# Optimization experiments

Measured on AMD Instinct MI355X. Metric: run time of the kernel, lower is better.

Reference implementation:

```python
import jax, jax.numpy as jnp
import numpy as np

N = 50000
E = 800000
FEAT, COND, HID, LAT = 64, 32, 64, 32


def gcn_conv(x, W, b, src, dst, n):
    xw = x @ W  # [N, out]
    deg = jnp.zeros((n,), xw.dtype).at[dst].add(1.0) + 1.0  # in-degree + self loop
    dinv = jax.lax.rsqrt(deg)
    coef = dinv[src] * dinv[dst]  # [E]
    msg = xw[src] * coef[:, None]  # gather + scale
    agg = jax.ops.segment_sum(msg, dst, num_segments=n)
    agg = agg + xw * (1.0 / deg)[:, None]  # self-loop contribution
    return agg + b


def setup_inputs() -> dict:
    key = jax.random.key(0)
    ks = jax.random.split(key, 12)
    s = 0.05
    return {
        "feature": jax.random.normal(ks[0], (N, FEAT), jnp.float32),
        "condition": jax.random.normal(ks[1], (N, COND), jnp.float32),
        "edge_index": jax.random.randint(ks[2], (2, E), 0, N, jnp.int64),
        "enc_i2h_W": jax.random.normal(ks[3], (FEAT + COND, HID), jnp.float32) * s,
        "enc_i2h_b": jnp.zeros((HID,), jnp.float32),
        "enc_mean_W": jax.random.normal(ks[4], (HID, LAT), jnp.float32) * s,
        "enc_mean_b": jnp.zeros((LAT,), jnp.float32),
        "enc_logvar_W": jax.random.normal(ks[5], (HID, LAT), jnp.float32) * s,
        "enc_logvar_b": jnp.zeros((LAT,), jnp.float32),
        "dec_i2h_W": jax.random.normal(ks[6], (LAT + COND, HID), jnp.float32) * s,
        "dec_i2h_b": jnp.zeros((HID,), jnp.float32),
        "dec_out_W": jax.random.normal(ks[7], (HID, FEAT), jnp.float32) * s,
        "dec_out_b": jnp.zeros((FEAT,), jnp.float32),
    }


def reference(feature, condition, edge_index,
              enc_i2h_W, enc_i2h_b, enc_mean_W, enc_mean_b,
              enc_logvar_W, enc_logvar_b,
              dec_i2h_W, dec_i2h_b, dec_out_W, dec_out_b):
    src, dst = edge_index[0], edge_index[1]
    n = feature.shape[0]
    # encoder
    x = jnp.concatenate([feature, condition], axis=1)
    h = jax.nn.relu(gcn_conv(x, enc_i2h_W, enc_i2h_b, src, dst, n))
    mean = gcn_conv(h, enc_mean_W, enc_mean_b, src, dst, n)
    logvar = gcn_conv(h, enc_logvar_W, enc_logvar_b, src, dst, n)
    noise = jax.random.normal(jax.random.key(42), logvar.shape, logvar.dtype)
    z = noise * jnp.exp(0.5 * logvar) + mean
    # decoder
    xd = jnp.concatenate([z, condition], axis=1)
    hd = jax.nn.relu(gcn_conv(xd, dec_i2h_W, dec_i2h_b, src, dst, n))
    out = gcn_conv(hd, dec_out_W, dec_out_b, src, dst, n)
    return (z, mean, logvar, out)
```

## Files before the change

### kernel.cpp

```cpp
#include <hip/hip_runtime.h>
#include <hip/hip_bf16.h>
#include <hip/hip_fp16.h>
#include <math.h>


static __device__ __forceinline__ unsigned rotl32(unsigned x, int d) {
  return (x << d) | (x >> (32 - d));
}

static __device__ __forceinline__ void threefry_0_42(unsigned& x0, unsigned& x1) {
  const unsigned ks0 = 0u, ks1 = 42u, ks2 = 0u ^ 42u ^ 0x1BD11BDAu;
  x0 += ks0; x1 += ks1;
#define TF_R(r) { x0 += x1; x1 = rotl32(x1, (r)); x1 ^= x0; }
  TF_R(13) TF_R(15) TF_R(26) TF_R(6)
  x0 += ks1; x1 += ks2 + 1u;
  TF_R(17) TF_R(29) TF_R(16) TF_R(24)
  x0 += ks2; x1 += ks0 + 2u;
  TF_R(13) TF_R(15) TF_R(26) TF_R(6)
  x0 += ks0; x1 += ks1 + 3u;
  TF_R(17) TF_R(29) TF_R(16) TF_R(24)
  x0 += ks1; x1 += ks2 + 4u;
  TF_R(13) TF_R(15) TF_R(26) TF_R(6)
  x0 += ks2; x1 += ks0 + 5u;
#undef TF_R
}

static __device__ __forceinline__ float erfinv_f(float u) {
  float w = -logf((1.0f - u) * (1.0f + u));
  float p;
  if (w < 5.0f) {
    w = w - 2.5f;
    p = 2.81022636e-08f;
    p = fmaf(p, w, 3.43273939e-07f);
    p = fmaf(p, w, -3.5233877e-06f);
    p = fmaf(p, w, -4.39150654e-06f);
    p = fmaf(p, w, 0.00021858087f);
    p = fmaf(p, w, -0.00125372503f);
    p = fmaf(p, w, -0.00417768164f);
    p = fmaf(p, w, 0.246640727f);
    p = fmaf(p, w, 1.50140941f);
  } else {
    w = sqrtf(w) - 3.0f;
    p = -0.000200214257f;
    p = fmaf(p, w, 0.000100950558f);
    p = fmaf(p, w, 0.00134934322f);
    p = fmaf(p, w, -0.00367342844f);
    p = fmaf(p, w, 0.00573950773f);
    p = fmaf(p, w, -0.0076224613f);
    p = fmaf(p, w, 0.00943887047f);
    p = fmaf(p, w, 1.00167406f);
    p = fmaf(p, w, 2.83297682f);
  }
  return p * u;
}

static __device__ __forceinline__ float jax_normal_at(unsigned j) {
  unsigned x0 = 0u, x1 = j;
  threefry_0_42(x0, x1);
  unsigned bits = x0 ^ x1;
  float f = __uint_as_float((bits >> 9) | 0x3f800000u) - 1.0f;
  float u = fmaf(f, 1.99999994f, -0.99999994f);
  return 1.41421356237f * erfinv_f(u);
}


__global__ void zero_i_kernel(int* __restrict__ p, int n) {
  int i = blockIdx.x * blockDim.x + threadIdx.x;
  if (i < n) p[i] = 0;
}

__global__ void degree_i_kernel(const int* __restrict__ dstI, int* __restrict__ cnt, int ne) {
  int e = blockIdx.x * blockDim.x + threadIdx.x;
  if (e < ne) atomicAdd(&cnt[dstI[e]], 1);
}

__global__ __launch_bounds__(256) void scan1_kernel(const int* __restrict__ cnt,
                                                    int* __restrict__ rowptr,
                                                    int* __restrict__ bsum, int n) {
  __shared__ int s[256];
  const int t = threadIdx.x;
  const int base = blockIdx.x * 1024 + t * 4;
  int v0, v1, v2, v3;
  if (base + 3 < n) {
    int4 v = *(const int4*)(cnt + base);
    v0 = v.x; v1 = v.y; v2 = v.z; v3 = v.w;
  } else {
    v0 = (base + 0 < n) ? cnt[base + 0] : 0;
    v1 = (base + 1 < n) ? cnt[base + 1] : 0;
    v2 = (base + 2 < n) ? cnt[base + 2] : 0;
    v3 = (base + 3 < n) ? cnt[base + 3] : 0;
  }
  int tot = v0 + v1 + v2 + v3;
  s[t] = tot;
  __syncthreads();
  for (int off = 1; off < 256; off <<= 1) {
    int x = (t >= off) ? s[t - off] : 0;
    __syncthreads();
    s[t] += x;
    __syncthreads();
  }
  int excl = s[t] - tot;
  if (t == 255) bsum[blockIdx.x] = s[t];
  if (base + 0 < n) rowptr[base + 0] = excl;
  if (base + 1 < n) rowptr[base + 1] = excl + v0;
  if (base + 2 < n) rowptr[base + 2] = excl + v0 + v1;
  if (base + 3 < n) rowptr[base + 3] = excl + v0 + v1 + v2;
}

__global__ __launch_bounds__(256) void scanP_kernel(int* __restrict__ bsum,
                                                    int* __restrict__ boff,
                                                    int nb, int* __restrict__ rowptr,
                                                    int n, int ne) {
  __shared__ int s[256];
  const int t = threadIdx.x;
  int v = (t < nb) ? bsum[t] : 0;
  s[t] = v;
  __syncthreads();
  for (int off = 1; off < 256; off <<= 1) {
    int x = (t >= off) ? s[t - off] : 0;
    __syncthreads();
    s[t] += x;
    __syncthreads();
  }
  if (t < nb) boff[t] = s[t] - v;
  if (t == 0) rowptr[n] = ne;
}

__global__ void scan2_kernel(int* __restrict__ rowptr, const int* __restrict__ boff,
                             int* __restrict__ cnt, float* __restrict__ dinv, int n) {
  int i = blockIdx.x * blockDim.x + threadIdx.x;
  if (i < n) {
    rowptr[i] += boff[i >> 10];
    float d = (float)cnt[i] + 1.0f;
    dinv[i] = 1.0f / sqrtf(d);
    cnt[i] = 0;
  }
}

__global__ void fill_kernel(const int* __restrict__ srcI, const int* __restrict__ dstI,
                            const int* __restrict__ rowptr, int* __restrict__ cnt,
                            unsigned short* __restrict__ ssrc, int ne) {
  int e = blockIdx.x * blockDim.x + threadIdx.x;
  if (e >= ne) return;
  int s = srcI[e], d = dstI[e];
  int pos = rowptr[d] + atomicAdd(&cnt[d], 1);
  ssrc[pos] = (unsigned short)s;
}

struct alignas(16) half8 { __half h[8]; };

template<int IN1, int IN2, bool DUALW>
__global__ __launch_bounds__(256) void gemm_kernel(
    const float* __restrict__ X1, const float* __restrict__ X2,
    const float* __restrict__ Wa, const float* __restrict__ Wb,
    const float* __restrict__ dinv, __half* __restrict__ Y, int n) {
  constexpr int IN = IN1 + IN2;
  constexpr int IP = IN + 4;
  __shared__ float xs[128 * IP];
  __shared__ float ws[IN * 64];

  const int tid = threadIdx.x;
  const int base = blockIdx.x * 128;

  for (int i = tid; i < IN * 64; i += 256) {
    if (DUALW) {
      int k = i >> 6, c = i & 63;
      ws[i] = (c < 32) ? Wa[k * 32 + c] : Wb[k * 32 + (c - 32)];
    } else {
      ws[i] = Wa[i];
    }
  }
  for (int idx = tid; idx < 128 * (IN1 / 4); idx += 256) {
    int node = idx / (IN1 / 4);
    int k4 = (idx % (IN1 / 4)) * 4;
    int g = base + node;
    float4 v = (g < n) ? *(const float4*)(X1 + (size_t)g * IN1 + k4)
                       : make_float4(0.f, 0.f, 0.f, 0.f);
    *(float4*)&xs[node * IP + k4] = v;
  }
  if (IN2 > 0) {
    for (int idx = tid; idx < 128 * (IN2 / 4); idx += 256) {
      int node = idx / (IN2 / 4);
      int k4 = (idx % (IN2 / 4)) * 4;
      int g = base + node;
      float4 v = (g < n) ? *(const float4*)(X2 + (size_t)g * IN2 + k4)
                         : make_float4(0.f, 0.f, 0.f, 0.f);
      *(float4*)&xs[node * IP + IN1 + k4] = v;
    }
  }
  __syncthreads();

  const int c8 = (tid & 7) * 8;
  const int r4 = (tid >> 3) * 4;
  float acc[4][8];
#pragma unroll
  for (int i = 0; i < 4; ++i)
#pragma unroll
    for (int c = 0; c < 8; ++c) acc[i][c] = 0.0f;

#pragma unroll 2
  for (int kk = 0; kk < IN; kk += 4) {
    float4 xv[4];
    float4 wv[4][2];
#pragma unroll
    for (int i = 0; i < 4; ++i) xv[i] = *(const float4*)&xs[(r4 + i) * IP + kk];
#pragma unroll
    for (int j = 0; j < 4; ++j) {
      wv[j][0] = *(const float4*)&ws[(kk + j) * 64 + c8];
      wv[j][1] = *(const float4*)&ws[(kk + j) * 64 + c8 + 4];
    }
#pragma unroll
    for (int i = 0; i < 4; ++i) {
      const float* xi = (const float*)&xv[i];
#pragma unroll
      for (int j = 0; j < 4; ++j) {
        const float* wj = (const float*)&wv[j][0];
#pragma unroll
        for (int c = 0; c < 8; ++c) {
          acc[i][c] = fmaf(xi[j], wj[c], acc[i][c]);
        }
      }
    }
  }

#pragma unroll
  for (int i = 0; i < 4; ++i) {
    int g = base + r4 + i;
    if (g < n) {
      float dv = dinv[g];
      half8 o;
#pragma unroll
      for (int c = 0; c < 8; ++c) o.h[c] = __float2half(acc[i][c] * dv);
      *(half8*)&Y[(size_t)g * 64 + c8] = o;
    }
  }
}

template<int MODE>
__global__ __launch_bounds__(256) void gather_kernel(
    const int* __restrict__ rowptr, const unsigned short* __restrict__ ssrc,
    const __half* __restrict__ xwp, const float* __restrict__ dinv,
    const float* __restrict__ b0, const float* __restrict__ b1,
    float* __restrict__ out, int n) {
  const int node = (blockIdx.x * 256 + threadIdx.x) >> 6;
  const int lane = threadIdx.x & 63;
  if (node >= n) return;
  const int hf = lane >> 5;
  const int cl = lane & 31;

  float2 a1, a2, a3, a4;
  a2.x = a2.y = a3.x = a3.y = a4.x = a4.y = 0.f;
  {
    float2 f = __half22float2(((const __half2*)(xwp + (size_t)node * 64))[cl]);
    a1.x = hf ? 0.f : f.x;
    a1.y = hf ? 0.f : f.y;
  }

  const int beg = rowptr[node];
  const int end = rowptr[node + 1];
  for (int cbase = beg; cbase < end; cbase += 64) {
    int m = end - cbase; if (m > 64) m = 64;
    unsigned sv = (lane < m) ? (unsigned)ssrc[cbase + lane] : 0u;
    int k = 0;
    for (; k + 7 < m; k += 8) {
      unsigned sa = __shfl(sv, k + 0 + hf, 64);
      unsigned sb = __shfl(sv, k + 2 + hf, 64);
      unsigned sc = __shfl(sv, k + 4 + hf, 64);
      unsigned sd = __shfl(sv, k + 6 + hf, 64);
      float2 fa = __half22float2(((const __half2*)(xwp + (size_t)sa * 64))[cl]);
      float2 fb = __half22float2(((const __half2*)(xwp + (size_t)sb * 64))[cl]);
      float2 fc = __half22float2(((const __half2*)(xwp + (size_t)sc * 64))[cl]);
      float2 fd = __half22float2(((const __half2*)(xwp + (size_t)sd * 64))[cl]);
      a1.x += fa.x; a1.y += fa.y;
      a2.x += fb.x; a2.y += fb.y;
      a3.x += fc.x; a3.y += fc.y;
      a4.x += fd.x; a4.y += fd.y;
    }
    for (; k + 1 < m; k += 2) {
      unsigned sa = __shfl(sv, k + hf, 64);
      float2 fa = __half22float2(((const __half2*)(xwp + (size_t)sa * 64))[cl]);
      a1.x += fa.x; a1.y += fa.y;
    }
    if (k < m) {
      unsigned sa = __shfl(sv, k, 64);
      if (hf == 0) {
        float2 fa = __half22float2(((const __half2*)(xwp + (size_t)sa * 64))[cl]);
        a1.x += fa.x; a1.y += fa.y;
      }
    }
  }
  float2 acc;
  acc.x = (a1.x + a2.x) + (a3.x + a4.x);
  acc.y = (a1.y + a2.y) + (a3.y + a4.y);
  acc.x += __shfl(acc.x, lane ^ 32, 64);
  acc.y += __shfl(acc.y, lane ^ 32, 64);
  float dv = dinv[node];
  float vx = acc.x * dv, vy = acc.y * dv;

  if (hf != 0) return;

  const int c0 = 2 * cl;
  if (MODE == 0) {
    float2 o;
    o.x = fmaxf(vx + b0[c0], 0.0f);
    o.y = fmaxf(vy + b0[c0 + 1], 0.0f);
    ((float2*)(out + (size_t)node * 64))[cl] = o;
  } else if (MODE == 2) {
    float2 o;
    o.x = vx + b0[c0];
    o.y = vy + b0[c0 + 1];
    ((float2*)(out + (size_t)node * 64))[cl] = o;
  } else {
    float bx = (c0 < 32) ? b0[c0] : b1[c0 - 32];
    float by = (c0 + 1 < 32) ? b0[c0 + 1] : b1[c0 + 1 - 32];
    vx += bx; vy += by;
    float ox = __shfl(vx, lane + 16, 64);
    float oy = __shfl(vy, lane + 16, 64);
    const int NZ = n * 32;
    if (cl < 16) {
      int j = node * 32 + c0;
      float n0 = jax_normal_at((unsigned)j);
      float n1 = jax_normal_at((unsigned)(j + 1));
      out[j]     = fmaf(n0, expf(0.5f * ox), vx);
      out[j + 1] = fmaf(n1, expf(0.5f * oy), vy);
      out[NZ + j]     = vx;
      out[NZ + j + 1] = vy;
    } else {
      int j = node * 32 + (c0 - 32);
      out[2 * NZ + j]     = vx;
      out[2 * NZ + j + 1] = vy;
    }
  }
}


extern "C" void kernel_launch(void* const* d_in, const int* in_sizes, int n_in,
                              void* d_out, int out_size, void* d_ws, size_t ws_size,
                              hipStream_t stream) {
  const float* feat = (const float*)d_in[0];
  const float* cond = (const float*)d_in[1];
  const int*   eidx = (const int*)d_in[2];
  const float* W1  = (const float*)d_in[3];
  const float* b1  = (const float*)d_in[4];
  const float* Wm  = (const float*)d_in[5];
  const float* bm  = (const float*)d_in[6];
  const float* Wlv = (const float*)d_in[7];
  const float* blv = (const float*)d_in[8];
  const float* Wd  = (const float*)d_in[9];
  const float* bd  = (const float*)d_in[10];
  const float* Wo  = (const float*)d_in[11];
  const float* bo  = (const float*)d_in[12];

  const int n  = in_sizes[0] / 64;
  const int ne = in_sizes[2] / 2;
  const int* srcI = eidx;
  const int* dstI = eidx + ne;

  int*   cnt    = (int*)d_ws;
  int*   rowptr = cnt + n;
  int*   bsum   = rowptr + n + 1;
  int*   boff   = bsum + 256;
  float* dinv   = (float*)(boff + 256);
  __half* xwp   = (__half*)(dinv + n);
  float* h      = (float*)(xwp + (size_t)n * 64);
  unsigned short* ssrc = (unsigned short*)(h + (size_t)n * 64);

  float* dout   = (float*)d_out;
  float* zbuf   = dout;
  float* outbuf = dout + (size_t)3 * n * 32;

  const int BT = 256;
  auto blk = [](long long t) { return (int)((t + 255) / 256); };
  const int nb_n  = blk(n);
  const int nb_e  = blk(ne);
  const int nb_sc = (n + 1023) / 1024;
  const int nb_gw = blk((long long)n * 64);
  const int nb_g  = (n + 127) / 128;

  hipLaunchKernelGGL(zero_i_kernel, dim3(nb_n), dim3(BT), 0, stream, cnt, n);
  hipLaunchKernelGGL(degree_i_kernel, dim3(nb_e), dim3(BT), 0, stream, dstI, cnt, ne);
  hipLaunchKernelGGL(scan1_kernel, dim3(nb_sc), dim3(BT), 0, stream, cnt, rowptr, bsum, n);
  hipLaunchKernelGGL(scanP_kernel, dim3(1), dim3(BT), 0, stream, bsum, boff, nb_sc, rowptr, n, ne);
  hipLaunchKernelGGL(scan2_kernel, dim3(nb_n), dim3(BT), 0, stream, rowptr, boff, cnt, dinv, n);
  hipLaunchKernelGGL(fill_kernel, dim3(nb_e), dim3(BT), 0, stream,
                     srcI, dstI, rowptr, cnt, ssrc, ne);

  hipLaunchKernelGGL((gemm_kernel<64, 32, false>), dim3(nb_g), dim3(BT), 0, stream,
                     feat, cond, W1, nullptr, dinv, xwp, n);
  hipLaunchKernelGGL((gather_kernel<0>), dim3(nb_gw), dim3(BT), 0, stream,
                     rowptr, ssrc, xwp, dinv, b1, nullptr, h, n);

  hipLaunchKernelGGL((gemm_kernel<64, 0, true>), dim3(nb_g), dim3(BT), 0, stream,
                     h, nullptr, Wm, Wlv, dinv, xwp, n);
  hipLaunchKernelGGL((gather_kernel<1>), dim3(nb_gw), dim3(BT), 0, stream,
                     rowptr, ssrc, xwp, dinv, bm, blv, dout, n);

  hipLaunchKernelGGL((gemm_kernel<32, 32, false>), dim3(nb_g), dim3(BT), 0, stream,
                     zbuf, cond, Wd, nullptr, dinv, xwp, n);
  hipLaunchKernelGGL((gather_kernel<0>), dim3(nb_gw), dim3(BT), 0, stream,
                     rowptr, ssrc, xwp, dinv, bd, nullptr, h, n);

  hipLaunchKernelGGL((gemm_kernel<64, 0, false>), dim3(nb_g), dim3(BT), 0, stream,
                     h, nullptr, Wo, nullptr, dinv, xwp, n);
  hipLaunchKernelGGL((gather_kernel<2>), dim3(nb_gw), dim3(BT), 0, stream,
                     rowptr, ssrc, xwp, dinv, bo, nullptr, outbuf, n);
}
```

Measured before the change: 273.3 us.

## Use fp16 MFMA for node GEMMs and store hidden activations in fp16

Replaces the scalar FMA register-tiled GEMM with an MFMA 16x16x32 fp16 kernel. Inputs and a transposed weight tile are staged in LDS as fp16. The hidden activations h written by the ReLU gather are now stored as fp16, which halves their write and read traffic, and the next GEMM loads them directly. The output stores become scattered per-element half writes rather than 16-byte vectors, and inputs lose precision by being rounded to fp16. dinv is offset by 3 ints, likely to keep later buffers aligned for vector loads.

```diff
diff --git a/kernel.cpp b/kernel.cpp
--- a/kernel.cpp
+++ b/kernel.cpp
@@ -2,6 +2,10 @@
 #include <hip/hip_bf16.h>
 #include <hip/hip_fp16.h>
 #include <math.h>
+
+typedef _Float16 f16;
+typedef __attribute__((ext_vector_type(8))) _Float16 f16x8;
+typedef __attribute__((ext_vector_type(4))) float f32x4;
 
 
 static __device__ __forceinline__ unsigned rotl32(unsigned x, int d) {
@@ -147,36 +151,47 @@
   ssrc[pos] = (unsigned short)s;
 }
 
-struct alignas(16) half8 { __half h[8]; };
-
-template<int IN1, int IN2, bool DUALW>
-__global__ __launch_bounds__(256) void gemm_kernel(
-    const float* __restrict__ X1, const float* __restrict__ X2,
+template<int IN1, int IN2, bool X1HALF, bool DUALW>
+__global__ __launch_bounds__(256) void gemm_mfma_kernel(
+    const void* __restrict__ X1v, const float* __restrict__ X2,
     const float* __restrict__ Wa, const float* __restrict__ Wb,
     const float* __restrict__ dinv, __half* __restrict__ Y, int n) {
   constexpr int IN = IN1 + IN2;
-  constexpr int IP = IN + 4;
-  __shared__ float xs[128 * IP];
-  __shared__ float ws[IN * 64];
+  constexpr int IP = IN + 8;
+  __shared__ f16 xs[128 * IP];
+  __shared__ f16 wt[64 * IP];
 
   const int tid = threadIdx.x;
   const int base = blockIdx.x * 128;
 
   for (int i = tid; i < IN * 64; i += 256) {
-    if (DUALW) {
-      int k = i >> 6, c = i & 63;
-      ws[i] = (c < 32) ? Wa[k * 32 + c] : Wb[k * 32 + (c - 32)];
-    } else {
-      ws[i] = Wa[i];
-    }
-  }
-  for (int idx = tid; idx < 128 * (IN1 / 4); idx += 256) {
-    int node = idx / (IN1 / 4);
-    int k4 = (idx % (IN1 / 4)) * 4;
-    int g = base + node;
-    float4 v = (g < n) ? *(const float4*)(X1 + (size_t)g * IN1 + k4)
-                       : make_float4(0.f, 0.f, 0.f, 0.f);
-    *(float4*)&xs[node * IP + k4] = v;
+    int k = i >> 6, c = i & 63;
+    float w;
+    if (DUALW) w = (c < 32) ? Wa[k * 32 + c] : Wb[k * 32 + (c - 32)];
+    else       w = Wa[i];
+    wt[c * IP + k] = (f16)w;
+  }
+  if (X1HALF) {
+    const __half* X1 = (const __half*)X1v;
+    for (int idx = tid; idx < 128 * (IN1 / 8); idx += 256) {
+      int node = idx / (IN1 / 8);
+      int k8 = (idx % (IN1 / 8)) * 8;
+      int g = base + node;
+      f16x8 v = {};
+      if (g < n) v = *(const f16x8*)(X1 + (size_t)g * IN1 + k8);
+      *(f16x8*)&xs[node * IP + k8] = v;
+    }
+  } else {
+    const float* X1 = (const float*)X1v;
+    for (int idx = tid; idx < 128 * (IN1 / 4); idx += 256) {
+      int node = idx / (IN1 / 4);
+      int k4 = (idx % (IN1 / 4)) * 4;
+      int g = base + node;
+      float4 v = (g < n) ? *(const float4*)(X1 + (size_t)g * IN1 + k4)
+                         : make_float4(0.f, 0.f, 0.f, 0.f);
+      f16* p = &xs[node * IP + k4];
+      p[0] = (f16)v.x; p[1] = (f16)v.y; p[2] = (f16)v.z; p[3] = (f16)v.w;
+    }
   }
   if (IN2 > 0) {
     for (int idx = tid; idx < 128 * (IN2 / 4); idx += 256) {
@@ -185,53 +200,44 @@
       int g = base + node;
       float4 v = (g < n) ? *(const float4*)(X2 + (size_t)g * IN2 + k4)
                          : make_float4(0.f, 0.f, 0.f, 0.f);
-      *(float4*)&xs[node * IP + IN1 + k4] = v;
+      f16* p = &xs[node * IP + IN1 + k4];
+      p[0] = (f16)v.x; p[1] = (f16)v.y; p[2] = (f16)v.z; p[3] = (f16)v.w;
     }
   }
   __syncthreads();
 
-  const int c8 = (tid & 7) * 8;
-  const int r4 = (tid >> 3) * 4;
-  float acc[4][8];
+  const int wid  = tid >> 6;
+  const int lane = tid & 63;
+  const int l15  = lane & 15;
+  const int lk8  = (lane >> 4) * 8;
+
+  f32x4 acc[2][4] = {{{0.f,0.f,0.f,0.f}}};
+  constexpr int KB = IN / 32;
 #pragma unroll
-  for (int i = 0; i < 4; ++i)
+  for (int kb = 0; kb < KB; ++kb) {
+    const int k0 = kb * 32 + lk8;
+    f16x8 a0 = *(const f16x8*)&xs[(wid * 32 +      l15) * IP + k0];
+    f16x8 a1 = *(const f16x8*)&xs[(wid * 32 + 16 + l15) * IP + k0];
 #pragma unroll
-    for (int c = 0; c < 8; ++c) acc[i][c] = 0.0f;
-
-#pragma unroll 2
-  for (int kk = 0; kk < IN; kk += 4) {
-    float4 xv[4];
-    float4 wv[4][2];
+    for (int ct = 0; ct < 4; ++ct) {
+      f16x8 b = *(const f16x8*)&wt[(ct * 16 + l15) * IP + k0];
+      acc[0][ct] = __builtin_amdgcn_mfma_f32_16x16x32_f16(a0, b, acc[0][ct], 0, 0, 0);
+      acc[1][ct] = __builtin_amdgcn_mfma_f32_16x16x32_f16(a1, b, acc[1][ct], 0, 0, 0);
+    }
+  }
+
 #pragma unroll
-    for (int i = 0; i < 4; ++i) xv[i] = *(const float4*)&xs[(r4 + i) * IP + kk];
-#pragma unroll
-    for (int j = 0; j < 4; ++j) {
-      wv[j][0] = *(const float4*)&ws[(kk + j) * 64 + c8];
-      wv[j][1] = *(const float4*)&ws[(kk + j) * 64 + c8 + 4];
-    }
+  for (int rt = 0; rt < 2; ++rt) {
 #pragma unroll
     for (int i = 0; i < 4; ++i) {
-      const float* xi = (const float*)&xv[i];
+      int node = base + wid * 32 + rt * 16 + (lane >> 4) * 4 + i;
+      if (node < n) {
+        float dv = dinv[node];
 #pragma unroll
-      for (int j = 0; j < 4; ++j) {
-        const float* wj = (const float*)&wv[j][0];
-#pragma unroll
-        for (int c = 0; c < 8; ++c) {
-          acc[i][c] = fmaf(xi[j], wj[c], acc[i][c]);
+        for (int ct = 0; ct < 4; ++ct) {
+          Y[(size_t)node * 64 + ct * 16 + l15] = __float2half(acc[rt][ct][i] * dv);
         }
       }
-    }
-  }
-
-#pragma unroll
-  for (int i = 0; i < 4; ++i) {
-    int g = base + r4 + i;
-    if (g < n) {
-      float dv = dinv[g];
-      half8 o;
-#pragma unroll
-      for (int c = 0; c < 8; ++c) o.h[c] = __float2half(acc[i][c] * dv);
-      *(half8*)&Y[(size_t)g * 64 + c8] = o;
     }
   }
 }
@@ -241,7 +247,7 @@
     const int* __restrict__ rowptr, const unsigned short* __restrict__ ssrc,
     const __half* __restrict__ xwp, const float* __restrict__ dinv,
     const float* __restrict__ b0, const float* __restrict__ b1,
-    float* __restrict__ out, int n) {
+    void* __restrict__ outv, int n) {
   const int node = (blockIdx.x * 256 + threadIdx.x) >> 6;
   const int lane = threadIdx.x & 63;
   if (node >= n) return;
@@ -301,16 +307,17 @@
 
   const int c0 = 2 * cl;
   if (MODE == 0) {
-    float2 o;
-    o.x = fmaxf(vx + b0[c0], 0.0f);
-    o.y = fmaxf(vy + b0[c0 + 1], 0.0f);
-    ((float2*)(out + (size_t)node * 64))[cl] = o;
+    __half* out = (__half*)outv;
+    __half2 o = __floats2half2_rn(fmaxf(vx + b0[c0], 0.0f), fmaxf(vy + b0[c0 + 1], 0.0f));
+    ((__half2*)(out + (size_t)node * 64))[cl] = o;
   } else if (MODE == 2) {
+    float* out = (float*)outv;
     float2 o;
     o.x = vx + b0[c0];
     o.y = vy + b0[c0 + 1];
     ((float2*)(out + (size_t)node * 64))[cl] = o;
   } else {
+    float* out = (float*)outv;
     float bx = (c0 < 32) ? b0[c0] : b1[c0 - 32];
     float by = (c0 + 1 < 32) ? b0[c0 + 1] : b1[c0 + 1 - 32];
     vx += bx; vy += by;
@@ -360,9 +367,9 @@
   int*   rowptr = cnt + n;
   int*   bsum   = rowptr + n + 1;
   int*   boff   = bsum + 256;
-  float* dinv   = (float*)(boff + 256);
+  float* dinv   = (float*)(boff + 256 + 3);
   __half* xwp   = (__half*)(dinv + n);
-  float* h      = (float*)(xwp + (size_t)n * 64);
+  __half* h     = xwp + (size_t)n * 64;
   unsigned short* ssrc = (unsigned short*)(h + (size_t)n * 64);
 
   float* dout   = (float*)d_out;
@@ -385,22 +392,22 @@
   hipLaunchKernelGGL(fill_kernel, dim3(nb_e), dim3(BT), 0, stream,
                      srcI, dstI, rowptr, cnt, ssrc, ne);
 
-  hipLaunchKernelGGL((gemm_kernel<64, 32, false>), dim3(nb_g), dim3(BT), 0, stream,
+  hipLaunchKernelGGL((gemm_mfma_kernel<64, 32, false, false>), dim3(nb_g), dim3(BT), 0, stream,
                      feat, cond, W1, nullptr, dinv, xwp, n);
   hipLaunchKernelGGL((gather_kernel<0>), dim3(nb_gw), dim3(BT), 0, stream,
                      rowptr, ssrc, xwp, dinv, b1, nullptr, h, n);
 
-  hipLaunchKernelGGL((gemm_kernel<64, 0, true>), dim3(nb_g), dim3(BT), 0, stream,
+  hipLaunchKernelGGL((gemm_mfma_kernel<64, 0, true, true>), dim3(nb_g), dim3(BT), 0, stream,
                      h, nullptr, Wm, Wlv, dinv, xwp, n);
   hipLaunchKernelGGL((gather_kernel<1>), dim3(nb_gw), dim3(BT), 0, stream,
                      rowptr, ssrc, xwp, dinv, bm, blv, dout, n);
 
-  hipLaunchKernelGGL((gemm_kernel<32, 32, false>), dim3(nb_g), dim3(BT), 0, stream,
+  hipLaunchKernelGGL((gemm_mfma_kernel<32, 32, false, false>), dim3(nb_g), dim3(BT), 0, stream,
                      zbuf, cond, Wd, nullptr, dinv, xwp, n);
   hipLaunchKernelGGL((gather_kernel<0>), dim3(nb_gw), dim3(BT), 0, stream,
                      rowptr, ssrc, xwp, dinv, bd, nullptr, h, n);
 
-  hipLaunchKernelGGL((gemm_kernel<64, 0, false>), dim3(nb_g), dim3(BT), 0, stream,
+  hipLaunchKernelGGL((gemm_mfma_kernel<64, 0, true, false>), dim3(nb_g), dim3(BT), 0, stream,
                      h, nullptr, Wo, nullptr, dinv, xwp, n);
   hipLaunchKernelGGL((gather_kernel<2>), dim3(nb_gw), dim3(BT), 0, stream,
                      rowptr, ssrc, xwp, dinv, bo, nullptr, outbuf, n);
```

Result: faster. 248.0 us (-9.3%).
